# Kernel optimization log

Hardware: AMD Instinct MI355X
Metric: run time of the kernel (lower is better)

Reference implementation:

```python
import jax, jax.numpy as jnp
import numpy as np


def setup_inputs() -> dict:
    key = jax.random.key(0)
    k1, k2, k3 = jax.random.split(key, 3)
    B, D, T, DEPTH = 16384, 512, 64, 6
    x = jax.random.normal(k1, (B, D), dtype=jnp.float32)
    # per-tree learned params, stacked over the tree axis (num_trees)
    feature_selectors = jax.random.normal(k2, (T, DEPTH, D), dtype=jnp.float32)
    thresholds = jnp.zeros((T, DEPTH), dtype=jnp.float32)
    leaf_weights = jax.random.normal(k3, (T, 2 ** DEPTH, 1), dtype=jnp.float32)
    return {"x": x, "feature_selectors": feature_selectors,
            "thresholds": thresholds, "leaf_weights": leaf_weights}


def reference(x, feature_selectors, thresholds, leaf_weights):
    # x: [B, D]; feature_selectors: [T, depth, D]; thresholds: [T, depth]
    # leaf_weights: [T, 2^depth, 1]
    B = x.shape[0]
    T, depth, _ = feature_selectors.shape
    # all trees' split logits in one GEMM: [B, T, depth]
    logits = jnp.einsum('bi,tdi->btd', x, feature_selectors) - thresholds
    probs = jax.nn.sigmoid(logits)
    # probs_stack[..., 0] = p, probs_stack[..., 1] = 1 - p  -> [B, T, depth, 2]
    probs_stack = jnp.stack([probs, 1.0 - probs], axis=-1)
    # build leaf probabilities via repeated outer products over the depth axis
    leaf = probs_stack[:, :, 0]  # [B, T, 2]
    for d in range(1, depth):
        # [B, T, 2^d, 1] * [B, T, 1, 2] -> [B, T, 2^(d+1)]
        leaf = (leaf[..., :, None] * probs_stack[:, :, d][:, :, None, :]).reshape(B, T, -1)
    # per-tree leaf_probs @ weights, summed over trees -> [B, 1]
    out = jnp.einsum('btl,tlo->bo', leaf, leaf_weights)
    return out
```

## Files before the change

### kernel.cpp

```cpp
#include <hip/hip_runtime.h>


#define DD     512
#define NCOL   384
#define NDEPTH 6

typedef __bf16 bf16_t;
typedef __bf16 bf16x8 __attribute__((ext_vector_type(8)));
typedef float  f32x4  __attribute__((ext_vector_type(4)));

static __device__ __forceinline__ float b2f(unsigned int u16) {
  unsigned int t = u16 << 16;
  float f;
  __builtin_memcpy(&f, &t, 4);
  return f;
}

__global__ __launch_bounds__(256) void node_pack(const float* __restrict__ fsel,
                                                 const float* __restrict__ lw,
                                                 bf16_t* __restrict__ pk,
                                                 float* __restrict__ lwT)
{
  if (blockIdx.x < 96) {
    int tid  = blockIdx.x * 256 + threadIdx.x;
    int lane = tid & 63;
    int ksg  = (tid >> 6) & 15;
    int cf   = tid >> 10;
    int col  = cf * 16 + (lane & 15);
    int k    = ksg * 32 + (lane >> 4) * 8;
    float4 f0 = *reinterpret_cast<const float4*>(fsel + (size_t)col * DD + k);
    float4 f1 = *reinterpret_cast<const float4*>(fsel + (size_t)col * DD + k + 4);
    bf16x8 v;
    v[0] = (bf16_t)f0.x; v[1] = (bf16_t)f0.y; v[2] = (bf16_t)f0.z; v[3] = (bf16_t)f0.w;
    v[4] = (bf16_t)f1.x; v[5] = (bf16_t)f1.y; v[6] = (bf16_t)f1.z; v[7] = (bf16_t)f1.w;
    *reinterpret_cast<bf16x8*>(pk + (size_t)tid * 8) = v;
  } else {
    #pragma unroll
    for (int it = 0; it < 16; ++it) {
      int i = it * 256 + threadIdx.x;
      int t = i & 63, j = i >> 6;
      lwT[j * 64 + t] = lw[t * 64 + j];
    }
  }
}

__global__ __launch_bounds__(512, 2) void node_gemm(
    const float*  __restrict__ x,
    const bf16_t* __restrict__ pk,
    const float*  __restrict__ thr,
    bf16_t*       __restrict__ probs)
{
  __shared__ bf16_t xf[2][8192];

  const int tid  = threadIdx.x;
  const int lane = tid & 63;
  const int wv   = tid >> 6;
  const int rowblk = blockIdx.x * 64;
  const int srow = lane & 15;
  const int skg  = lane >> 4;

  bf16x8 breg[3][16];
  #pragma unroll
  for (int f = 0; f < 3; ++f) {
    #pragma unroll
    for (int ks = 0; ks < 16; ++ks) {
      breg[f][ks] = *reinterpret_cast<const bf16x8*>(
          pk + ((size_t)(((wv * 3 + f) * 16 + ks) * 64) + lane) * 8);
    }
  }

  float th[3];
  #pragma unroll
  for (int f = 0; f < 3; ++f) th[f] = thr[wv * 48 + f * 16 + (lane & 15)];

  float4 st[4];

  #define ISSUE_LOADS(t)                                                        \
    do {                                                                        \
      const float* base_ = x + (size_t)(rowblk + (t) * 16 + srow) * DD + skg*8; \
      st[0] = *reinterpret_cast<const float4*>(base_ + wv * 32);                \
      st[1] = *reinterpret_cast<const float4*>(base_ + wv * 32 + 4);            \
      st[2] = *reinterpret_cast<const float4*>(base_ + (wv + 8) * 32);          \
      st[3] = *reinterpret_cast<const float4*>(base_ + (wv + 8) * 32 + 4);      \
    } while (0)

  #define WRITE_LDS(buf)                                                        \
    do {                                                                        \
      bf16x8 v0_, v1_;                                                          \
      v0_[0]=(bf16_t)st[0].x; v0_[1]=(bf16_t)st[0].y;                           \
      v0_[2]=(bf16_t)st[0].z; v0_[3]=(bf16_t)st[0].w;                           \
      v0_[4]=(bf16_t)st[1].x; v0_[5]=(bf16_t)st[1].y;                           \
      v0_[6]=(bf16_t)st[1].z; v0_[7]=(bf16_t)st[1].w;                           \
      v1_[0]=(bf16_t)st[2].x; v1_[1]=(bf16_t)st[2].y;                           \
      v1_[2]=(bf16_t)st[2].z; v1_[3]=(bf16_t)st[2].w;                           \
      v1_[4]=(bf16_t)st[3].x; v1_[5]=(bf16_t)st[3].y;                           \
      v1_[6]=(bf16_t)st[3].z; v1_[7]=(bf16_t)st[3].w;                           \
      *reinterpret_cast<bf16x8*>(&xf[buf][(wv * 64 + lane) * 8])       = v0_;   \
      *reinterpret_cast<bf16x8*>(&xf[buf][((wv + 8) * 64 + lane) * 8]) = v1_;   \
    } while (0)

  ISSUE_LOADS(0);
  WRITE_LDS(0);
  ISSUE_LOADS(1);
  asm volatile("s_waitcnt lgkmcnt(0)" ::: "memory");
  __builtin_amdgcn_s_barrier();

  #pragma unroll
  for (int t = 0; t < 4; ++t) {
    const int buf = t & 1;
    if (t < 3) WRITE_LDS(buf ^ 1);
    if (t < 2) ISSUE_LOADS(t + 2);

    f32x4 acc[3];
    #pragma unroll
    for (int f = 0; f < 3; ++f) acc[f] = (f32x4){0.f, 0.f, 0.f, 0.f};

    #pragma unroll
    for (int ks = 0; ks < 16; ++ks) {
      bf16x8 a = *reinterpret_cast<const bf16x8*>(&xf[buf][(ks * 64 + lane) * 8]);
      acc[0] = __builtin_amdgcn_mfma_f32_16x16x32_bf16(a, breg[0][ks], acc[0], 0, 0, 0);
      acc[1] = __builtin_amdgcn_mfma_f32_16x16x32_bf16(a, breg[1][ks], acc[1], 0, 0, 0);
      acc[2] = __builtin_amdgcn_mfma_f32_16x16x32_bf16(a, breg[2][ks], acc[2], 0, 0, 0);
    }

    #pragma unroll
    for (int f = 0; f < 3; ++f) {
      const int col = wv * 48 + f * 16 + (lane & 15);
      #pragma unroll
      for (int r = 0; r < 4; ++r) {
        const int row = rowblk + t * 16 + (lane >> 4) * 4 + r;
        float z = acc[f][r] - th[f];
        float p = 1.0f / (1.0f + __expf(-z));
        probs[(size_t)row * NCOL + col] = (bf16_t)p;
      }
    }

    if (t < 3) {
      asm volatile("s_waitcnt lgkmcnt(0)" ::: "memory");
      __builtin_amdgcn_s_barrier();
    }
  }
  #undef ISSUE_LOADS
  #undef WRITE_LDS
}

__global__ __launch_bounds__(256) void node_fold(
    const bf16_t* __restrict__ probs,
    const float*  __restrict__ lwT,
    float*        __restrict__ out)
{
  const int lane = threadIdx.x & 63;
  const int wv   = threadIdx.x >> 6;
  const int rowbase = blockIdx.x * 16 + wv * 4;

  float w[64];
  #pragma unroll
  for (int j = 0; j < 64; ++j) w[j] = lwT[j * 64 + lane];

  #pragma unroll
  for (int rr = 0; rr < 4; ++rr) {
    const unsigned int* pr =
        reinterpret_cast<const unsigned int*>(probs + (size_t)(rowbase + rr) * NCOL) + lane * 3;
    unsigned int d0 = pr[0], d1 = pr[1], d2 = pr[2];
    float p[NDEPTH];
    p[0] = b2f(d0 & 0xffffu); p[1] = b2f(d0 >> 16);
    p[2] = b2f(d1 & 0xffffu); p[3] = b2f(d1 >> 16);
    p[4] = b2f(d2 & 0xffffu); p[5] = b2f(d2 >> 16);

    float v[32];
    #pragma unroll
    for (int j = 0; j < 32; ++j) v[j] = fmaf(p[5], w[2*j] - w[2*j+1], w[2*j+1]);
    #pragma unroll
    for (int j = 0; j < 16; ++j) v[j] = fmaf(p[4], v[2*j] - v[2*j+1], v[2*j+1]);
    #pragma unroll
    for (int j = 0; j < 8;  ++j) v[j] = fmaf(p[3], v[2*j] - v[2*j+1], v[2*j+1]);
    #pragma unroll
    for (int j = 0; j < 4;  ++j) v[j] = fmaf(p[2], v[2*j] - v[2*j+1], v[2*j+1]);
    #pragma unroll
    for (int j = 0; j < 2;  ++j) v[j] = fmaf(p[1], v[2*j] - v[2*j+1], v[2*j+1]);
    float tv = fmaf(p[0], v[0] - v[1], v[1]);

    #pragma unroll
    for (int off = 32; off; off >>= 1) tv += __shfl_xor(tv, off, 64);
    if (lane == 0) out[rowbase + rr] = tv;
  }
}

extern "C" void kernel_launch(void* const* d_in, const int* in_sizes, int n_in,
                              void* d_out, int out_size, void* d_ws, size_t ws_size,
                              hipStream_t stream) {
  const float* x    = (const float*)d_in[0];
  const float* fsel = (const float*)d_in[1];
  const float* thr  = (const float*)d_in[2];
  const float* lw   = (const float*)d_in[3];
  float* out = (float*)d_out;

  char* ws = (char*)d_ws;
  bf16_t* pk    = (bf16_t*)ws;
  float*  lwT   = (float*)(ws + 393216);
  bf16_t* probs = (bf16_t*)(ws + 409600);

  const int B = in_sizes[0] / DD;

  node_pack<<<dim3(97), dim3(256), 0, stream>>>(fsel, lw, pk, lwT);
  node_gemm<<<dim3(B / 64), dim3(512), 0, stream>>>(x, pk, thr, probs);
  node_fold<<<dim3(B / 16), dim3(256), 0, stream>>>(probs, lwT, out);
}
```

Before: 31.11 us.

## Fuse node GEMM and leaf fold via LDS probabilities, drop lwT transpose

Merges the GEMM+sigmoid kernel with the leaf-fold kernel: probabilities for the 64-row block are written to shared memory rather than global, and each wave then folds 8 rows with leaf weights read directly (vectorized, no transpose) from the input. This removes a kernel launch, the global round-trip of the bf16 probability matrix, and the lwT transpose. In exchange the x staging drops from double to single buffering with an extra barrier per tile, and LDS use grows to about 64 KB per block, which may reduce occupancy.

```diff
diff --git a/kernel.cpp b/kernel.cpp
--- a/kernel.cpp
+++ b/kernel.cpp
@@ -17,40 +17,31 @@
 }
 
 __global__ __launch_bounds__(256) void node_pack(const float* __restrict__ fsel,
-                                                 const float* __restrict__ lw,
-                                                 bf16_t* __restrict__ pk,
-                                                 float* __restrict__ lwT)
+                                                 bf16_t* __restrict__ pk)
 {
-  if (blockIdx.x < 96) {
-    int tid  = blockIdx.x * 256 + threadIdx.x;
-    int lane = tid & 63;
-    int ksg  = (tid >> 6) & 15;
-    int cf   = tid >> 10;
-    int col  = cf * 16 + (lane & 15);
-    int k    = ksg * 32 + (lane >> 4) * 8;
-    float4 f0 = *reinterpret_cast<const float4*>(fsel + (size_t)col * DD + k);
-    float4 f1 = *reinterpret_cast<const float4*>(fsel + (size_t)col * DD + k + 4);
-    bf16x8 v;
-    v[0] = (bf16_t)f0.x; v[1] = (bf16_t)f0.y; v[2] = (bf16_t)f0.z; v[3] = (bf16_t)f0.w;
-    v[4] = (bf16_t)f1.x; v[5] = (bf16_t)f1.y; v[6] = (bf16_t)f1.z; v[7] = (bf16_t)f1.w;
-    *reinterpret_cast<bf16x8*>(pk + (size_t)tid * 8) = v;
-  } else {
-    #pragma unroll
-    for (int it = 0; it < 16; ++it) {
-      int i = it * 256 + threadIdx.x;
-      int t = i & 63, j = i >> 6;
-      lwT[j * 64 + t] = lw[t * 64 + j];
-    }
-  }
+  int tid  = blockIdx.x * 256 + threadIdx.x;
+  int lane = tid & 63;
+  int ksg  = (tid >> 6) & 15;
+  int cf   = tid >> 10;
+  int col  = cf * 16 + (lane & 15);
+  int k    = ksg * 32 + (lane >> 4) * 8;
+  float4 f0 = *reinterpret_cast<const float4*>(fsel + (size_t)col * DD + k);
+  float4 f1 = *reinterpret_cast<const float4*>(fsel + (size_t)col * DD + k + 4);
+  bf16x8 v;
+  v[0] = (bf16_t)f0.x; v[1] = (bf16_t)f0.y; v[2] = (bf16_t)f0.z; v[3] = (bf16_t)f0.w;
+  v[4] = (bf16_t)f1.x; v[5] = (bf16_t)f1.y; v[6] = (bf16_t)f1.z; v[7] = (bf16_t)f1.w;
+  *reinterpret_cast<bf16x8*>(pk + (size_t)tid * 8) = v;
 }
 
-__global__ __launch_bounds__(512, 2) void node_gemm(
+__global__ __launch_bounds__(512, 2) void node_fused(
     const float*  __restrict__ x,
     const bf16_t* __restrict__ pk,
     const float*  __restrict__ thr,
-    bf16_t*       __restrict__ probs)
+    const float*  __restrict__ lw,
+    float*        __restrict__ out)
 {
-  __shared__ bf16_t xf[2][8192];
+  __shared__ bf16_t xf[8192];
+  __shared__ bf16_t pr[64 * NCOL];
 
   const int tid  = threadIdx.x;
   const int lane = tid & 63;
@@ -84,7 +75,7 @@
       st[3] = *reinterpret_cast<const float4*>(base_ + (wv + 8) * 32 + 4);      \
     } while (0)
 
-  #define WRITE_LDS(buf)                                                        \
+  #define WRITE_LDS()                                                           \
     do {                                                                        \
       bf16x8 v0_, v1_;                                                          \
       v0_[0]=(bf16_t)st[0].x; v0_[1]=(bf16_t)st[0].y;                           \
@@ -95,21 +86,18 @@
       v1_[2]=(bf16_t)st[2].z; v1_[3]=(bf16_t)st[2].w;                           \
       v1_[4]=(bf16_t)st[3].x; v1_[5]=(bf16_t)st[3].y;                           \
       v1_[6]=(bf16_t)st[3].z; v1_[7]=(bf16_t)st[3].w;                           \
-      *reinterpret_cast<bf16x8*>(&xf[buf][(wv * 64 + lane) * 8])       = v0_;   \
-      *reinterpret_cast<bf16x8*>(&xf[buf][((wv + 8) * 64 + lane) * 8]) = v1_;   \
+      *reinterpret_cast<bf16x8*>(&xf[(wv * 64 + lane) * 8])       = v0_;        \
+      *reinterpret_cast<bf16x8*>(&xf[((wv + 8) * 64 + lane) * 8]) = v1_;        \
     } while (0)
 
   ISSUE_LOADS(0);
-  WRITE_LDS(0);
-  ISSUE_LOADS(1);
-  asm volatile("s_waitcnt lgkmcnt(0)" ::: "memory");
-  __builtin_amdgcn_s_barrier();
 
   #pragma unroll
   for (int t = 0; t < 4; ++t) {
-    const int buf = t & 1;
-    if (t < 3) WRITE_LDS(buf ^ 1);
-    if (t < 2) ISSUE_LOADS(t + 2);
+    WRITE_LDS();
+    if (t < 3) ISSUE_LOADS(t + 1);
+    asm volatile("s_waitcnt lgkmcnt(0)" ::: "memory");
+    __builtin_amdgcn_s_barrier();
 
     f32x4 acc[3];
     #pragma unroll
@@ -117,7 +105,7 @@
 
     #pragma unroll
     for (int ks = 0; ks < 16; ++ks) {
-      bf16x8 a = *reinterpret_cast<const bf16x8*>(&xf[buf][(ks * 64 + lane) * 8]);
+      bf16x8 a = *reinterpret_cast<const bf16x8*>(&xf[(ks * 64 + lane) * 8]);
       acc[0] = __builtin_amdgcn_mfma_f32_16x16x32_bf16(a, breg[0][ks], acc[0], 0, 0, 0);
       acc[1] = __builtin_amdgcn_mfma_f32_16x16x32_bf16(a, breg[1][ks], acc[1], 0, 0, 0);
       acc[2] = __builtin_amdgcn_mfma_f32_16x16x32_bf16(a, breg[2][ks], acc[2], 0, 0, 0);
@@ -128,40 +116,32 @@
       const int col = wv * 48 + f * 16 + (lane & 15);
       #pragma unroll
       for (int r = 0; r < 4; ++r) {
-        const int row = rowblk + t * 16 + (lane >> 4) * 4 + r;
+        const int row = t * 16 + (lane >> 4) * 4 + r;
         float z = acc[f][r] - th[f];
         float p = 1.0f / (1.0f + __expf(-z));
-        probs[(size_t)row * NCOL + col] = (bf16_t)p;
+        pr[row * NCOL + col] = (bf16_t)p;
       }
     }
 
-    if (t < 3) {
-      asm volatile("s_waitcnt lgkmcnt(0)" ::: "memory");
-      __builtin_amdgcn_s_barrier();
-    }
+    asm volatile("s_waitcnt lgkmcnt(0)" ::: "memory");
+    __builtin_amdgcn_s_barrier();
   }
   #undef ISSUE_LOADS
   #undef WRITE_LDS
-}
-
-__global__ __launch_bounds__(256) void node_fold(
-    const bf16_t* __restrict__ probs,
-    const float*  __restrict__ lwT,
-    float*        __restrict__ out)
-{
-  const int lane = threadIdx.x & 63;
-  const int wv   = threadIdx.x >> 6;
-  const int rowbase = blockIdx.x * 16 + wv * 4;
 
   float w[64];
   #pragma unroll
-  for (int j = 0; j < 64; ++j) w[j] = lwT[j * 64 + lane];
+  for (int j = 0; j < 16; ++j) {
+    float4 f = *reinterpret_cast<const float4*>(lw + (size_t)lane * 64 + j * 4);
+    w[4*j] = f.x; w[4*j+1] = f.y; w[4*j+2] = f.z; w[4*j+3] = f.w;
+  }
 
   #pragma unroll
-  for (int rr = 0; rr < 4; ++rr) {
-    const unsigned int* pr =
-        reinterpret_cast<const unsigned int*>(probs + (size_t)(rowbase + rr) * NCOL) + lane * 3;
-    unsigned int d0 = pr[0], d1 = pr[1], d2 = pr[2];
+  for (int rr = 0; rr < 8; ++rr) {
+    const int row = wv * 8 + rr;
+    const unsigned int* prow =
+        reinterpret_cast<const unsigned int*>(pr + row * NCOL) + lane * 3;
+    unsigned int d0 = prow[0], d1 = prow[1], d2 = prow[2];
     float p[NDEPTH];
     p[0] = b2f(d0 & 0xffffu); p[1] = b2f(d0 >> 16);
     p[2] = b2f(d1 & 0xffffu); p[3] = b2f(d1 >> 16);
@@ -182,7 +162,7 @@
 
     #pragma unroll
     for (int off = 32; off; off >>= 1) tv += __shfl_xor(tv, off, 64);
-    if (lane == 0) out[rowbase + rr] = tv;
+    if (lane == 0) out[rowblk + row] = tv;
   }
 }
 
@@ -195,14 +175,10 @@
   const float* lw   = (const float*)d_in[3];
   float* out = (float*)d_out;
 
-  char* ws = (char*)d_ws;
-  bf16_t* pk    = (bf16_t*)ws;
-  float*  lwT   = (float*)(ws + 393216);
-  bf16_t* probs = (bf16_t*)(ws + 409600);
+  bf16_t* pk = (bf16_t*)d_ws;
 
   const int B = in_sizes[0] / DD;
 
-  node_pack<<<dim3(97), dim3(256), 0, stream>>>(fsel, lw, pk, lwT);
-  node_gemm<<<dim3(B / 64), dim3(512), 0, stream>>>(x, pk, thr, probs);
-  node_fold<<<dim3(B / 16), dim3(256), 0, stream>>>(probs, lwT, out);
+  node_pack<<<dim3(96), dim3(256), 0, stream>>>(fsel, pk);
+  node_fused<<<dim3(B / 64), dim3(512), 0, stream>>>(x, pk, thr, lw, out);
 }
```

After: 31.56 us. About the same (+1.4%).
